# Kernel tuning notes

Hardware: AMD Instinct MI355X
Metric: run time of the kernel (lower is better)

The kernel has to match this reference:

```python
import jax, jax.numpy as jnp
import numpy as np

BLOCK = 32  # GGML Q8_0 block size


def setup_inputs() -> dict:
    key = jax.random.key(0)
    k1, k2, k3, k4 = jax.random.split(key, 4)
    B, S, I, O = 2, 2048, 4096, 16384
    x = jax.random.normal(k1, (B, S, I), dtype=jnp.float32)
    # Q8_0-style signed 8-bit quants stored as int32 for portability
    qweight = jax.random.randint(k2, (O, I), -127, 128, dtype=jnp.int32)
    # one positive fp scale per 32-element block
    scales = jax.random.uniform(k3, (O, I // BLOCK), dtype=jnp.float32,
                                minval=0.005, maxval=0.02)
    bias = jax.random.normal(k4, (O,), dtype=jnp.float32) * 0.01
    return {"x": x, "qweight": qweight, "scales": scales, "bias": bias}


def reference(x, qweight, scales, bias):
    # dequantize_tensor: per-block scale * int8 quants -> full precision weight
    O, I = qweight.shape
    w = qweight.astype(x.dtype).reshape(O, I // BLOCK, BLOCK) * scales[:, :, None]
    w = w.reshape(O, I)  # [O, I]
    # Linear forward: y = x @ W^T + b
    return jnp.einsum('bsd,od->bso', x, w) + bias
```

## Files before the change

kernel.cpp:

```cpp
#include <hip/hip_runtime.h>
#include <cstdint>
#include <cstddef>

#define M_DIM 4096
#define N_DIM 16384
#define K_DIM 4096
#define QBLK 32

constexpr int BM = 128, BN = 128, BK = 64;
constexpr int NT = K_DIM / BK;

typedef __bf16 bf16x8 __attribute__((ext_vector_type(8)));
typedef float  f32x4  __attribute__((ext_vector_type(4)));
typedef unsigned short u16x8 __attribute__((ext_vector_type(8)));

__device__ __forceinline__ unsigned short f2bf(float f) {
    unsigned int x = __builtin_bit_cast(unsigned int, f);
    x += 0x7fffu + ((x >> 16) & 1u);
    return (unsigned short)(x >> 16);
}

__device__ __forceinline__ void gload16(const void* g, void* l) {
    __builtin_amdgcn_global_load_lds((__attribute__((address_space(1))) unsigned int*)(g),
                                     (__attribute__((address_space(3))) unsigned int*)(l),
                                     16, 0, 0);
}

__global__ __launch_bounds__(256) void cvt_x_kernel(const float* __restrict__ x,
                                                    unsigned short* __restrict__ o) {
    const size_t total = (size_t)M_DIM * K_DIM / 8;
    for (size_t i = (size_t)blockIdx.x * 256 + threadIdx.x; i < total;
         i += (size_t)gridDim.x * 256) {
        const float4* src = (const float4*)(x + i * 8);
        float4 a0 = src[0], a1 = src[1];
        u16x8 v;
        v[0] = f2bf(a0.x); v[1] = f2bf(a0.y); v[2] = f2bf(a0.z); v[3] = f2bf(a0.w);
        v[4] = f2bf(a1.x); v[5] = f2bf(a1.y); v[6] = f2bf(a1.z); v[7] = f2bf(a1.w);
        *(u16x8*)(o + i * 8) = v;
    }
}

__global__ __launch_bounds__(256) void dequant_w_kernel(const int* __restrict__ q,
                                                        const float* __restrict__ s,
                                                        unsigned short* __restrict__ o) {
    const size_t total = (size_t)N_DIM * K_DIM / 8;
    for (size_t i = (size_t)blockIdx.x * 256 + threadIdx.x; i < total;
         i += (size_t)gridDim.x * 256) {
        const int4* src = (const int4*)(q + i * 8);
        int4 q0 = src[0], q1 = src[1];
        float sc = s[i >> 2];
        u16x8 v;
        v[0] = f2bf((float)q0.x * sc); v[1] = f2bf((float)q0.y * sc);
        v[2] = f2bf((float)q0.z * sc); v[3] = f2bf((float)q0.w * sc);
        v[4] = f2bf((float)q1.x * sc); v[5] = f2bf((float)q1.y * sc);
        v[6] = f2bf((float)q1.z * sc); v[7] = f2bf((float)q1.w * sc);
        *(u16x8*)(o + i * 8) = v;
    }
}

template <bool FUSED>
__global__ __launch_bounds__(256, 2) void gemm_kernel(
    const unsigned short* __restrict__ Abf, const unsigned short* __restrict__ Bbf,
    const float* __restrict__ Xf, const int* __restrict__ Qw, const float* __restrict__ Sc,
    const float* __restrict__ bias, float* __restrict__ out) {

    __shared__ char smem[2 * 32768];

    const int t  = threadIdx.x;
    const int l  = t & 63;
    const int w  = t >> 6;
    const int wm = w >> 1, wn = w & 1;
    const int rowA0 = blockIdx.y * BM;
    const int colB0 = blockIdx.x * BN;

    const int lr   = l >> 3;
    const int sXor = (l & 7) ^ lr;

    const char* aSrc[4]; const char* bSrc[4];
    const float* aSrcF[4]; const int* bSrcQ[4]; const float* bSrcS[4];
    if constexpr (!FUSED) {
        #pragma unroll
        for (int j = 0; j < 4; ++j) {
            int c  = w * 4 + j;
            int ra = rowA0 + c * 8 + lr;
            int rb = colB0 + c * 8 + lr;
            aSrc[j] = (const char*)Abf + (size_t)ra * (K_DIM * 2) + (size_t)sXor * 16;
            bSrc[j] = (const char*)Bbf + (size_t)rb * (K_DIM * 2) + (size_t)sXor * 16;
        }
    } else {
        #pragma unroll
        for (int j = 0; j < 4; ++j) {
            int c  = w * 4 + j;
            int ra = rowA0 + c * 8 + lr;
            int rb = colB0 + c * 8 + lr;
            aSrcF[j] = Xf + (size_t)ra * K_DIM + sXor * 8;
            bSrcQ[j] = Qw + (size_t)rb * K_DIM + sXor * 8;
            bSrcS[j] = Sc + (size_t)rb * (K_DIM / QBLK) + (sXor >> 2);
        }
    }

    const int lrow = l & 15;
    const int l47  = l >> 4;
    const int lx   = l & 7;
    const unsigned raB0 = (unsigned)((wm * 64 + lrow) * 128 + ((l47 ^ lx) * 16));
    const unsigned raB1 = (unsigned)((wm * 64 + lrow) * 128 + (((4 | l47) ^ lx) * 16));
    const unsigned rbB0 = (unsigned)(16384 + (wn * 64 + lrow) * 128 + ((l47 ^ lx) * 16));
    const unsigned rbB1 = (unsigned)(16384 + (wn * 64 + lrow) * 128 + (((4 | l47) ^ lx) * 16));

    float fA[4][8]; int qB[4][8]; float sB[4];

    auto stage_direct = [&](int bsel) {
        #pragma unroll
        for (int j = 0; j < 4; ++j) {
            gload16(aSrc[j], &smem[bsel * 32768 + (w * 4 + j) * 1024]);
            aSrc[j] += BK * 2;
        }
        #pragma unroll
        for (int j = 0; j < 4; ++j) {
            gload16(bSrc[j], &smem[bsel * 32768 + 16384 + (w * 4 + j) * 1024]);
            bSrc[j] += BK * 2;
        }
    };
    auto stage_fused_load = [&]() {
        #pragma unroll
        for (int j = 0; j < 4; ++j) {
            float4 a0 = ((const float4*)aSrcF[j])[0];
            float4 a1 = ((const float4*)aSrcF[j])[1];
            fA[j][0] = a0.x; fA[j][1] = a0.y; fA[j][2] = a0.z; fA[j][3] = a0.w;
            fA[j][4] = a1.x; fA[j][5] = a1.y; fA[j][6] = a1.z; fA[j][7] = a1.w;
            aSrcF[j] += BK;
            int4 b0 = ((const int4*)bSrcQ[j])[0];
            int4 b1 = ((const int4*)bSrcQ[j])[1];
            qB[j][0] = b0.x; qB[j][1] = b0.y; qB[j][2] = b0.z; qB[j][3] = b0.w;
            qB[j][4] = b1.x; qB[j][5] = b1.y; qB[j][6] = b1.z; qB[j][7] = b1.w;
            bSrcQ[j] += BK;
            sB[j] = *bSrcS[j];
            bSrcS[j] += BK / QBLK;
        }
    };
    auto stage_fused_write = [&](int bsel) {
        #pragma unroll
        for (int j = 0; j < 4; ++j) {
            u16x8 va, vb;
            #pragma unroll
            for (int e = 0; e < 8; ++e) va[e] = f2bf(fA[j][e]);
            #pragma unroll
            for (int e = 0; e < 8; ++e) vb[e] = f2bf((float)qB[j][e] * sB[j]);
            *(u16x8*)(&smem[bsel * 32768 + (w * 4 + j) * 1024 + l * 16]) = va;
            *(u16x8*)(&smem[bsel * 32768 + 16384 + (w * 4 + j) * 1024 + l * 16]) = vb;
        }
    };

    f32x4 acc[4][4] = {};

    if constexpr (!FUSED) { stage_direct(0); }
    else { stage_fused_load(); stage_fused_write(0); }
    __syncthreads();

    int bsel = 0;
    for (int kt = 0; kt < NT; ++kt) {
        const bool pre = (kt + 1 < NT);
        if constexpr (!FUSED) { if (pre) stage_direct(bsel ^ 1); }
        else { if (pre) stage_fused_load(); }

        const unsigned boff = (unsigned)(bsel * 32768);
        #pragma unroll
        for (int kk = 0; kk < 2; ++kk) {
            bf16x8 av[4], bv[4];
            const unsigned ra = (kk ? raB1 : raB0) + boff;
            const unsigned rb = (kk ? rbB1 : rbB0) + boff;
            #pragma unroll
            for (int mf = 0; mf < 4; ++mf) av[mf] = *(const bf16x8*)(&smem[ra + mf * 2048]);
            #pragma unroll
            for (int nf = 0; nf < 4; ++nf) bv[nf] = *(const bf16x8*)(&smem[rb + nf * 2048]);
            #pragma unroll
            for (int mf = 0; mf < 4; ++mf)
                #pragma unroll
                for (int nf = 0; nf < 4; ++nf)
                    acc[mf][nf] = __builtin_amdgcn_mfma_f32_16x16x32_bf16(
                        av[mf], bv[nf], acc[mf][nf], 0, 0, 0);
        }

        if constexpr (FUSED) { if (pre) stage_fused_write(bsel ^ 1); }
        __syncthreads();
        bsel ^= 1;
    }

    const int orow0 = rowA0 + wm * 64 + l47 * 4;
    const int ocol0 = colB0 + wn * 64 + lrow;
    #pragma unroll
    for (int nf = 0; nf < 4; ++nf) {
        const float bv = bias[ocol0 + nf * 16];
        #pragma unroll
        for (int mf = 0; mf < 4; ++mf) {
            f32x4 v = acc[mf][nf];
            #pragma unroll
            for (int j = 0; j < 4; ++j) {
                const int r = orow0 + mf * 16 + j;
                out[(size_t)r * N_DIM + (ocol0 + nf * 16)] = v[j] + bv;
            }
        }
    }
}

extern "C" void kernel_launch(void* const* d_in, const int* in_sizes, int n_in,
                              void* d_out, int out_size, void* d_ws, size_t ws_size,
                              hipStream_t stream) {
    const float* x    = (const float*)d_in[0];
    const int*   qw   = (const int*)d_in[1];
    const float* sc   = (const float*)d_in[2];
    const float* bias = (const float*)d_in[3];
    float* out = (float*)d_out;

    const size_t need = ((size_t)M_DIM * K_DIM + (size_t)N_DIM * K_DIM) * 2;
    dim3 grid(N_DIM / BN, M_DIM / BM);

    if (ws_size >= need) {
        unsigned short* xb = (unsigned short*)d_ws;
        unsigned short* wb = xb + (size_t)M_DIM * K_DIM;
        cvt_x_kernel<<<dim3(1024), dim3(256), 0, stream>>>(x, xb);
        dequant_w_kernel<<<dim3(2048), dim3(256), 0, stream>>>(qw, sc, wb);
        gemm_kernel<false><<<grid, dim3(256), 0, stream>>>(xb, wb, nullptr, nullptr, nullptr,
                                                           bias, out);
    } else {
        gemm_kernel<true><<<grid, dim3(256), 0, stream>>>(nullptr, nullptr, x, qw, sc,
                                                          bias, out);
    }
}
```

Baseline: 1.032 ms.

## Replace bf16 GEMM with 256x256-tile, 8-wave, quarter-pipelined kernel

The unfused GEMM path now uses 256x256 output tiles with 512 threads and 128 KB of double-buffered LDS. Each K step is split into four sub-quadrant MFMA phases, with global-to-LDS loads interleaved under explicit barriers, waitcnt and setprio. Block IDs are remapped for L2 locality, and the convert/dequant kernels get larger grids. The goal is more data reuse per byte loaded and better overlap of memory with MFMA, at the cost of a complex hand-scheduled pipeline, high register use and lower occupancy.

```diff
diff --git a/kernel.cpp b/kernel.cpp
--- a/kernel.cpp
+++ b/kernel.cpp
@@ -6,9 +6,6 @@
 #define N_DIM 16384
 #define K_DIM 4096
 #define QBLK 32
-
-constexpr int BM = 128, BN = 128, BK = 64;
-constexpr int NT = K_DIM / BK;
 
 typedef __bf16 bf16x8 __attribute__((ext_vector_type(8)));
 typedef float  f32x4  __attribute__((ext_vector_type(4)));
@@ -58,87 +55,175 @@
     }
 }
 
-template <bool FUSED>
-__global__ __launch_bounds__(256, 2) void gemm_kernel(
+__global__ __launch_bounds__(512, 2) void gemm256(
     const unsigned short* __restrict__ Abf, const unsigned short* __restrict__ Bbf,
-    const float* __restrict__ Xf, const int* __restrict__ Qw, const float* __restrict__ Sc,
     const float* __restrict__ bias, float* __restrict__ out) {
 
-    __shared__ char smem[2 * 32768];
+    __shared__ char smem[131072];
 
     const int t  = threadIdx.x;
     const int l  = t & 63;
     const int w  = t >> 6;
+    const int wm = w >> 2;
+    const int wn = w & 3;
+
+    const int bid = blockIdx.y * 64 + blockIdx.x;
+    const int wg  = (bid & 7) * 128 + (bid >> 3);
+    const int bx  = wg & 63;
+    const int by  = wg >> 6;
+    const int tileM = by * 256;
+    const int tileN = bx * 256;
+
+    const int sr = w * 8 + (l >> 3);
+    const int cs = (l & 7) ^ (l >> 3);
+    const char* aP = (const char*)Abf + (size_t)(tileM + sr) * (K_DIM * 2) + cs * 16;
+    const char* bP = (const char*)Bbf + (size_t)(tileN + sr) * (K_DIM * 2) + cs * 16;
+    const int wq = w * 1024;
+
+    const int lrow = l & 15, l47 = l >> 4;
+    const int sw = lrow & 7;
+    const unsigned c0 = (unsigned)((l47 ^ sw) * 16);
+    const unsigned c1 = (unsigned)(((4 + l47) ^ sw) * 16);
+    const unsigned offA0 = (unsigned)((wm * 64 + lrow) * 128) + c0;
+    const unsigned offA1 = (unsigned)((wm * 64 + lrow) * 128) + c1;
+    const unsigned offB0 = (unsigned)((wn * 32 + lrow) * 128) + c0;
+    const unsigned offB1 = (unsigned)((wn * 32 + lrow) * 128) + c1;
+
+    bf16x8 avr[4][2];
+    bf16x8 bvr[2][2][2];
+    f32x4  acc[2][4][2][2] = {};
+
+#define ST_A(H, KT, DB) do { \
+    const char* g_ = aP + (size_t)(H) * 1048576u + (unsigned)(KT) * 128u; \
+    char* d_ = smem + (DB) * 65536 + (H) * 16384 + wq; \
+    gload16(g_, d_); gload16(g_ + 524288, d_ + 8192); } while (0)
+
+#define ST_B(H, KT, DB) do { \
+    const char* g_ = bP + (size_t)(H) * 1048576u + (unsigned)(KT) * 128u; \
+    char* d_ = smem + (DB) * 65536 + 32768 + (H) * 16384 + wq; \
+    gload16(g_, d_); gload16(g_ + 8192 * 64, d_ + 8192); } while (0)
+
+#define RD_A(DB, MH) do { \
+    const char* b_ = smem + (DB) * 65536 + (MH) * 16384; \
+    _Pragma("unroll") for (int mf_ = 0; mf_ < 4; ++mf_) { \
+        avr[mf_][0] = *(const bf16x8*)(b_ + offA0 + mf_ * 2048); \
+        avr[mf_][1] = *(const bf16x8*)(b_ + offA1 + mf_ * 2048); } } while (0)
+
+#define RD_B(DB, NH) do { \
+    const char* b_ = smem + (DB) * 65536 + 32768 + (NH) * 16384; \
+    _Pragma("unroll") for (int nf_ = 0; nf_ < 2; ++nf_) { \
+        bvr[NH][nf_][0] = *(const bf16x8*)(b_ + offB0 + nf_ * 2048); \
+        bvr[NH][nf_][1] = *(const bf16x8*)(b_ + offB1 + nf_ * 2048); } } while (0)
+
+#define MMQ(MH, NH) do { __builtin_amdgcn_s_setprio(1); \
+    _Pragma("unroll") for (int mf_ = 0; mf_ < 4; ++mf_) \
+    _Pragma("unroll") for (int nf_ = 0; nf_ < 2; ++nf_) \
+    _Pragma("unroll") for (int kk_ = 0; kk_ < 2; ++kk_) \
+        acc[MH][mf_][NH][nf_] = __builtin_amdgcn_mfma_f32_16x16x32_bf16( \
+            avr[mf_][kk_], bvr[NH][nf_][kk_], acc[MH][mf_][NH][nf_], 0, 0, 0); \
+    __builtin_amdgcn_s_setprio(0); } while (0)
+
+#define BAR __builtin_amdgcn_s_barrier()
+#define LGKM do { asm volatile("s_waitcnt lgkmcnt(0)" ::: "memory"); \
+                  __builtin_amdgcn_sched_barrier(0); } while (0)
+#define VMC(N) asm volatile("s_waitcnt vmcnt(" #N ")" ::: "memory")
+
+    ST_A(0, 0, 0); ST_A(1, 0, 0); ST_B(0, 0, 0); ST_B(1, 0, 0);
+    ST_A(0, 1, 1); ST_B(0, 1, 1);
+    VMC(4); BAR;
+
+    for (int i = 0; i < 32; ++i) {
+        const int k0 = 2 * i;
+        const int ka = (k0 + 1) & 63;
+        const int kb = (k0 + 2) & 63;
+        const int kc = (k0 + 3) & 63;
+        RD_A(0, 0); RD_B(0, 0); ST_A(1, ka, 1); BAR; LGKM; MMQ(0, 0); BAR;
+        RD_B(0, 1);             ST_B(1, ka, 1); BAR; LGKM; MMQ(0, 1); BAR;
+        RD_A(0, 1);             ST_A(0, kb, 0); BAR; LGKM; MMQ(1, 0); BAR;
+                                ST_B(0, kb, 0); BAR;       MMQ(1, 1); VMC(4); BAR;
+        RD_A(1, 0); RD_B(1, 0); ST_A(1, kb, 0); BAR; LGKM; MMQ(0, 0); BAR;
+        RD_B(1, 1);             ST_B(1, kb, 0); BAR; LGKM; MMQ(0, 1); BAR;
+        RD_A(1, 1);             ST_A(0, kc, 1); BAR; LGKM; MMQ(1, 0); BAR;
+                                ST_B(0, kc, 1); BAR;       MMQ(1, 1); VMC(4); BAR;
+    }
+
+    VMC(0);
+
+    #pragma unroll
+    for (int mh = 0; mh < 2; ++mh)
+    #pragma unroll
+    for (int nh = 0; nh < 2; ++nh)
+    #pragma unroll
+    for (int nf = 0; nf < 2; ++nf) {
+        const int col = tileN + nh * 128 + wn * 32 + nf * 16 + lrow;
+        const float bv = bias[col];
+        #pragma unroll
+        for (int mf = 0; mf < 4; ++mf) {
+            const int row0 = tileM + mh * 128 + wm * 64 + mf * 16 + l47 * 4;
+            f32x4 v = acc[mh][mf][nh][nf];
+            #pragma unroll
+            for (int j = 0; j < 4; ++j)
+                out[(size_t)(row0 + j) * N_DIM + col] = v[j] + bv;
+        }
+    }
+#undef ST_A
+#undef ST_B
+#undef RD_A
+#undef RD_B
+#undef MMQ
+#undef BAR
+#undef LGKM
+#undef VMC
+}
+
+__global__ __launch_bounds__(256, 2) void gemm_fused(
+    const float* __restrict__ Xf, const int* __restrict__ Qw, const float* __restrict__ Sc,
+    const float* __restrict__ bias, float* __restrict__ out) {
+
+    __shared__ char smem[2 * 32768];
+    const int t = threadIdx.x;
+    const int l = t & 63;
+    const int w = t >> 6;
     const int wm = w >> 1, wn = w & 1;
-    const int rowA0 = blockIdx.y * BM;
-    const int colB0 = blockIdx.x * BN;
-
-    const int lr   = l >> 3;
+    const int rowA0 = blockIdx.y * 128;
+    const int colB0 = blockIdx.x * 128;
+
+    const int lr = l >> 3;
     const int sXor = (l & 7) ^ lr;
 
-    const char* aSrc[4]; const char* bSrc[4];
     const float* aSrcF[4]; const int* bSrcQ[4]; const float* bSrcS[4];
-    if constexpr (!FUSED) {
-        #pragma unroll
-        for (int j = 0; j < 4; ++j) {
-            int c  = w * 4 + j;
-            int ra = rowA0 + c * 8 + lr;
-            int rb = colB0 + c * 8 + lr;
-            aSrc[j] = (const char*)Abf + (size_t)ra * (K_DIM * 2) + (size_t)sXor * 16;
-            bSrc[j] = (const char*)Bbf + (size_t)rb * (K_DIM * 2) + (size_t)sXor * 16;
-        }
-    } else {
-        #pragma unroll
-        for (int j = 0; j < 4; ++j) {
-            int c  = w * 4 + j;
-            int ra = rowA0 + c * 8 + lr;
-            int rb = colB0 + c * 8 + lr;
-            aSrcF[j] = Xf + (size_t)ra * K_DIM + sXor * 8;
-            bSrcQ[j] = Qw + (size_t)rb * K_DIM + sXor * 8;
-            bSrcS[j] = Sc + (size_t)rb * (K_DIM / QBLK) + (sXor >> 2);
-        }
-    }
-
-    const int lrow = l & 15;
-    const int l47  = l >> 4;
-    const int lx   = l & 7;
+    #pragma unroll
+    for (int j = 0; j < 4; ++j) {
+        int c = w * 4 + j;
+        aSrcF[j] = Xf + (size_t)(rowA0 + c * 8 + lr) * K_DIM + sXor * 8;
+        bSrcQ[j] = Qw + (size_t)(colB0 + c * 8 + lr) * K_DIM + sXor * 8;
+        bSrcS[j] = Sc + (size_t)(colB0 + c * 8 + lr) * (K_DIM / QBLK) + (sXor >> 2);
+    }
+
+    const int lrow = l & 15, l47 = l >> 4, lx = l & 7;
     const unsigned raB0 = (unsigned)((wm * 64 + lrow) * 128 + ((l47 ^ lx) * 16));
     const unsigned raB1 = (unsigned)((wm * 64 + lrow) * 128 + (((4 | l47) ^ lx) * 16));
     const unsigned rbB0 = (unsigned)(16384 + (wn * 64 + lrow) * 128 + ((l47 ^ lx) * 16));
     const unsigned rbB1 = (unsigned)(16384 + (wn * 64 + lrow) * 128 + (((4 | l47) ^ lx) * 16));
 
     float fA[4][8]; int qB[4][8]; float sB[4];
-
-    auto stage_direct = [&](int bsel) {
-        #pragma unroll
-        for (int j = 0; j < 4; ++j) {
-            gload16(aSrc[j], &smem[bsel * 32768 + (w * 4 + j) * 1024]);
-            aSrc[j] += BK * 2;
-        }
-        #pragma unroll
-        for (int j = 0; j < 4; ++j) {
-            gload16(bSrc[j], &smem[bsel * 32768 + 16384 + (w * 4 + j) * 1024]);
-            bSrc[j] += BK * 2;
-        }
-    };
-    auto stage_fused_load = [&]() {
+    auto load_s = [&]() {
         #pragma unroll
         for (int j = 0; j < 4; ++j) {
             float4 a0 = ((const float4*)aSrcF[j])[0];
             float4 a1 = ((const float4*)aSrcF[j])[1];
             fA[j][0] = a0.x; fA[j][1] = a0.y; fA[j][2] = a0.z; fA[j][3] = a0.w;
             fA[j][4] = a1.x; fA[j][5] = a1.y; fA[j][6] = a1.z; fA[j][7] = a1.w;
-            aSrcF[j] += BK;
+            aSrcF[j] += 64;
             int4 b0 = ((const int4*)bSrcQ[j])[0];
             int4 b1 = ((const int4*)bSrcQ[j])[1];
             qB[j][0] = b0.x; qB[j][1] = b0.y; qB[j][2] = b0.z; qB[j][3] = b0.w;
             qB[j][4] = b1.x; qB[j][5] = b1.y; qB[j][6] = b1.z; qB[j][7] = b1.w;
-            bSrcQ[j] += BK;
-            sB[j] = *bSrcS[j];
-            bSrcS[j] += BK / QBLK;
+            bSrcQ[j] += 64;
+            sB[j] = *bSrcS[j]; bSrcS[j] += 2;
         }
     };
-    auto stage_fused_write = [&](int bsel) {
+    auto write_s = [&](int bsel) {
         #pragma unroll
         for (int j = 0; j < 4; ++j) {
             u16x8 va, vb;
@@ -152,17 +237,12 @@
     };
 
     f32x4 acc[4][4] = {};
-
-    if constexpr (!FUSED) { stage_direct(0); }
-    else { stage_fused_load(); stage_fused_write(0); }
+    load_s(); write_s(0);
     __syncthreads();
-
     int bsel = 0;
-    for (int kt = 0; kt < NT; ++kt) {
-        const bool pre = (kt + 1 < NT);
-        if constexpr (!FUSED) { if (pre) stage_direct(bsel ^ 1); }
-        else { if (pre) stage_fused_load(); }
-
+    for (int kt = 0; kt < 64; ++kt) {
+        const bool pre = (kt + 1 < 64);
+        if (pre) load_s();
         const unsigned boff = (unsigned)(bsel * 32768);
         #pragma unroll
         for (int kk = 0; kk < 2; ++kk) {
@@ -180,12 +260,10 @@
                     acc[mf][nf] = __builtin_amdgcn_mfma_f32_16x16x32_bf16(
                         av[mf], bv[nf], acc[mf][nf], 0, 0, 0);
         }
-
-        if constexpr (FUSED) { if (pre) stage_fused_write(bsel ^ 1); }
+        if (pre) write_s(bsel ^ 1);
         __syncthreads();
         bsel ^= 1;
     }
-
     const int orow0 = rowA0 + wm * 64 + l47 * 4;
     const int ocol0 = colB0 + wn * 64 + lrow;
     #pragma unroll
@@ -195,10 +273,8 @@
         for (int mf = 0; mf < 4; ++mf) {
             f32x4 v = acc[mf][nf];
             #pragma unroll
-            for (int j = 0; j < 4; ++j) {
-                const int r = orow0 + mf * 16 + j;
-                out[(size_t)r * N_DIM + (ocol0 + nf * 16)] = v[j] + bv;
-            }
+            for (int j = 0; j < 4; ++j)
+                out[(size_t)(orow0 + mf * 16 + j) * N_DIM + (ocol0 + nf * 16)] = v[j] + bv;
         }
     }
 }
@@ -213,17 +289,13 @@
     float* out = (float*)d_out;
 
     const size_t need = ((size_t)M_DIM * K_DIM + (size_t)N_DIM * K_DIM) * 2;
-    dim3 grid(N_DIM / BN, M_DIM / BM);
-
     if (ws_size >= need) {
         unsigned short* xb = (unsigned short*)d_ws;
         unsigned short* wb = xb + (size_t)M_DIM * K_DIM;
-        cvt_x_kernel<<<dim3(1024), dim3(256), 0, stream>>>(x, xb);
-        dequant_w_kernel<<<dim3(2048), dim3(256), 0, stream>>>(qw, sc, wb);
-        gemm_kernel<false><<<grid, dim3(256), 0, stream>>>(xb, wb, nullptr, nullptr, nullptr,
-                                                           bias, out);
+        cvt_x_kernel<<<dim3(2048), dim3(256), 0, stream>>>(x, xb);
+        dequant_w_kernel<<<dim3(4096), dim3(256), 0, stream>>>(qw, sc, wb);
+        gemm256<<<dim3(64, 16), dim3(512), 0, stream>>>(xb, wb, bias, out);
     } else {
-        gemm_kernel<true><<<grid, dim3(256), 0, stream>>>(nullptr, nullptr, x, qw, sc,
-                                                          bias, out);
-    }
-}
+        gemm_fused<<<dim3(128, 32), dim3(256), 0, stream>>>(x, qw, sc, bias, out);
+    }
+}
```

Result: faster. 923.7 us (-10.5%).
